# Optimization experiments

Measured on AMD Instinct MI355X. Metric: run time of the kernel, lower is better.

The kernel has to match this reference:

```python
import jax, jax.numpy as jnp
import numpy as np

N_TF, N_GENES, W, FANIN, B = 1024, 20000, 4, 16, 128
M = N_GENES * W  # middle width = 80000


def _build_edges(rng):
    # layer 1: each of the M per-gene nodes draws FANIN random TF inputs
    out1 = np.repeat(np.arange(M, dtype=np.int32), FANIN)
    in1 = rng.integers(0, N_TF, size=M * FANIN).astype(np.int32)
    in1[-1] = N_TF - 1  # ensure full input dim is touched
    # layer 2: dense WxW block per gene (node i of gene g sees all W nodes of gene g)
    out2 = np.repeat(np.arange(M, dtype=np.int32), W)
    gene = np.arange(M, dtype=np.int32) // W
    in2 = (gene[:, None] * W + np.arange(W, dtype=np.int32)[None, :]).reshape(-1)
    # layer 3: each gene output sums its W nodes
    out3 = np.repeat(np.arange(N_GENES, dtype=np.int32), W)
    in3 = np.arange(M, dtype=np.int32)
    return out1, in1, out2, in2, out3, in3


def setup_inputs() -> dict:
    key = jax.random.key(0)
    ks = jax.random.split(key, 7)
    rng = np.random.default_rng(0)
    out1, in1, out2, in2, out3, in3 = _build_edges(rng)
    scale1 = 1.0 / np.sqrt(FANIN)
    scale2 = 1.0 / np.sqrt(W)
    return {
        "features": jax.random.normal(ks[0], (B, N_TF), jnp.float32),
        "w1": jax.random.normal(ks[1], (out1.shape[0],), jnp.float32) * scale1,
        "b1": jax.random.normal(ks[2], (M,), jnp.float32) * 0.01,
        "w2": jax.random.normal(ks[3], (out2.shape[0],), jnp.float32) * scale2,
        "b2": jax.random.normal(ks[4], (M,), jnp.float32) * 0.01,
        "w3": jax.random.normal(ks[5], (out3.shape[0],), jnp.float32) * scale2,
        "b3": jax.random.normal(ks[6], (N_GENES,), jnp.float32) * 0.01,
        "out1": jnp.asarray(out1), "in1": jnp.asarray(in1),
        "out2": jnp.asarray(out2), "in2": jnp.asarray(in2),
        "out3": jnp.asarray(out3), "in3": jnp.asarray(in3),
    }


def _sparse_linear(x, w, b, out_idx, in_idx):
    # x: [B, n_in]; per-edge gather-multiply-scatter, y[b, o] = sum_e w_e * x[b, in_e] + b_o
    contrib = x.T[in_idx] * w[:, None]                      # [nnz, B]
    y = jax.ops.segment_sum(contrib, out_idx, num_segments=b.shape[0])  # [n_out, B]
    return y.T + b


def reference(features, w1, b1, w2, b2, w3, b3, out1, in1, out2, in2, out3, in3):
    h = jnp.tanh(_sparse_linear(features, w1, b1, out1, in1))
    h = jnp.tanh(_sparse_linear(h, w2, b2, out2, in2))
    return _sparse_linear(h, w3, b3, out3, in3)  # [B, N_GENES]
```

## Files before the change

### kernel.cpp

```cpp
#include <hip/hip_runtime.h>
#include <hip/hip_fp16.h>

#define N_TF    1024
#define N_GENES 20000
#define WW      4
#define FANIN   16
#define BATCH   128
#define EPG     (WW * FANIN)
#define NNZ1    (N_GENES * EPG)

#define GPB      16
#define NTHREADS 1024
#define NBLK     (N_GENES / GPB)
#define YROW     (BATCH + 2)

typedef unsigned int uint32;

__device__ __forceinline__ float2 fast_tanh2(float a, float b) {
    const float ta = __expf(2.0f * a);
    const float tb = __expf(2.0f * b);
    const float da = ta + 1.0f;
    const float db = tb + 1.0f;
    const float r  = __builtin_amdgcn_rcpf(da * db);
    return make_float2(fmaf(-2.0f * db, r, 1.0f),
                       fmaf(-2.0f * da, r, 1.0f));
}

__global__ __launch_bounds__(256) void transpose_cvt_kernel(
    const float* __restrict__ in, __half* __restrict__ out)
{
    __shared__ float tile[32][33];
    const int bx = blockIdx.x;
    const int by = blockIdx.y;
    const int tx = threadIdx.x;
    const int ty = threadIdx.y;
#pragma unroll
    for (int k = 0; k < 32; k += 8)
        tile[ty + k][tx] = in[(by * 32 + ty + k) * N_TF + bx * 32 + tx];
    __syncthreads();
    const int b = by * 32 + tx;
#pragma unroll
    for (int k = 0; k < 32; k += 8) {
        const int tf = bx * 32 + ty + k;
        out[tf * BATCH + b] = __float2half(tile[tx][ty + k]);
    }
}

__global__ __launch_bounds__(NTHREADS, 4) void fused_kernel(
    const __half* __restrict__ xh,
    const int*    __restrict__ in1,
    const float*  __restrict__ w1,
    const float*  __restrict__ b1,
    const float*  __restrict__ w2,
    const float*  __restrict__ b2,
    const float*  __restrict__ w3,
    const float*  __restrict__ b3,
    float*        __restrict__ out)
{
    __shared__ float yt[GPB * YROW];

    const int tid  = threadIdx.x;
    const int wid  = __builtin_amdgcn_readfirstlane(tid >> 6);
    const int lane = tid & 63;
    const int g    = blockIdx.x * GPB + wid;
    const int voff = lane << 2;
    const char* xb = (const char*)xh;

    const uint4*  __restrict__ ig = (const uint4*)(in1 + g * EPG);
    const float4* __restrict__ wg = (const float4*)(w1 + g * EPG);

    __half2 acc[WW];
    const __half2 hz = __float2half2_rn(0.0f);
#pragma unroll
    for (int i = 0; i < WW; ++i) acc[i] = hz;

#pragma unroll
    for (int half = 0; half < 2; ++half) {
        uint32 idx[32];
        float  wsc[32];
#pragma unroll
        for (int k = 0; k < 8; ++k) {
            const uint4  iq = ig[half * 8 + k];
            const float4 wq = wg[half * 8 + k];
            idx[k * 4 + 0] = iq.x;  idx[k * 4 + 1] = iq.y;
            idx[k * 4 + 2] = iq.z;  idx[k * 4 + 3] = iq.w;
            wsc[k * 4 + 0] = wq.x;  wsc[k * 4 + 1] = wq.y;
            wsc[k * 4 + 2] = wq.z;  wsc[k * 4 + 3] = wq.w;
        }
        __half2 xv[32];
#pragma unroll
        for (int t = 0; t < 32; ++t)
            xv[t] = *(const __half2*)(xb + (((size_t)idx[t]) << 8) + voff);
#pragma unroll
        for (int t = 0; t < 32; ++t) {
            const __half2 wd = __float2half2_rn(wsc[t]);
            const int tt = half * 32 + t;
            acc[tt >> 4] = __hfma2(wd, xv[t], acc[tt >> 4]);
        }
    }

    float2 h1[WW];
#pragma unroll
    for (int i = 0; i < WW; ++i) {
        const float  bb = b1[g * WW + i];
        const float2 af = __half22float2(acc[i]);
        h1[i] = fast_tanh2(af.x + bb, af.y + bb);
    }

    float2 h2[WW];
#pragma unroll
    for (int i = 0; i < WW; ++i) {
        const float4 w  = *(const float4*)(w2 + g * 16 + i * 4);
        const float  bb = b2[g * WW + i];
        const float sx = bb + w.x * h1[0].x + w.y * h1[1].x
                            + w.z * h1[2].x + w.w * h1[3].x;
        const float sy = bb + w.x * h1[0].y + w.y * h1[1].y
                            + w.z * h1[2].y + w.w * h1[3].y;
        h2[i] = fast_tanh2(sx, sy);
    }

    const float4 wv3 = *(const float4*)(w3 + g * 4);
    const float  bv  = b3[g];
    const float yx = bv + wv3.x * h2[0].x + wv3.y * h2[1].x
                        + wv3.z * h2[2].x + wv3.w * h2[3].x;
    const float yy = bv + wv3.x * h2[0].y + wv3.y * h2[1].y
                        + wv3.z * h2[2].y + wv3.w * h2[3].y;

    float2* ytw = (float2*)(yt + wid * YROW);
    ytw[lane] = make_float2(yx, yy);

    __syncthreads();

    const int g0 = blockIdx.x * GPB;
#pragma unroll
    for (int it = 0; it < (BATCH * GPB) / NTHREADS; ++it) {
        const int idx = it * NTHREADS + tid;
        const int gq  = idx & (GPB - 1);
        const int b   = idx >> 4;
        out[b * N_GENES + g0 + gq] = yt[gq * YROW + b];
    }
}

extern "C" void kernel_launch(void* const* d_in, const int* in_sizes, int n_in,
                              void* d_out, int out_size, void* d_ws, size_t ws_size,
                              hipStream_t stream)
{
    const float* features = (const float*)d_in[0];
    const float* w1 = (const float*)d_in[1];
    const float* b1 = (const float*)d_in[2];
    const float* w2 = (const float*)d_in[3];
    const float* b2 = (const float*)d_in[4];
    const float* w3 = (const float*)d_in[5];
    const float* b3 = (const float*)d_in[6];
    const int*   in1 = (const int*)d_in[8];
    float* out = (float*)d_out;

    __half* xh = (__half*)d_ws;

    hipLaunchKernelGGL(transpose_cvt_kernel, dim3(32, 4), dim3(32, 8), 0, stream,
                       features, xh);
    hipLaunchKernelGGL(fused_kernel, dim3(NBLK), dim3(NTHREADS), 0, stream,
                       xh, in1, w1, b1, w2, b2, w3, b3, out);
}
```

Measured before the change: 112.1 us.

## Stage half-batch feature table in LDS and gather from shared memory

The feature matrix is split into two batch halves in the transposed fp16 layout. Each block copies one half (128 KB) into LDS and processes about 78 genes in a persistent loop over waves. Each wave handles two edges per instruction by splitting its lanes into two 32-lane groups and combines the partial sums with a cross-lane shuffle. This replaces random global/L2 gathers with LDS gathers. In exchange it adds a per-block 128 KB copy (512 blocks means 64 MB of total LDS fill traffic) and limits occupancy to one block per CU, which reduces latency hiding.

Measured after the change: 138.7 us. +23.7%, slower.

```diff
diff --git a/kernel.cpp b/kernel.cpp
--- a/kernel.cpp
+++ b/kernel.cpp
@@ -6,13 +6,17 @@
 #define WW      4
 #define FANIN   16
 #define BATCH   128
+#define HALF_B  64
 #define EPG     (WW * FANIN)
-#define NNZ1    (N_GENES * EPG)
 
-#define GPB      16
 #define NTHREADS 1024
-#define NBLK     (N_GENES / GPB)
-#define YROW     (BATCH + 2)
+#define NWAVES   16
+#define NBLK     512
+#define MAXG     80
+#define YROW     65
+#define XH_BYTES (N_TF * HALF_B * 2)
+#define YT_BYTES (MAXG * YROW * 4)
+#define LDS_BYTES (XH_BYTES + YT_BYTES)
 
 typedef unsigned int uint32;
 
@@ -38,16 +42,18 @@
     for (int k = 0; k < 32; k += 8)
         tile[ty + k][tx] = in[(by * 32 + ty + k) * N_TF + bx * 32 + tx];
     __syncthreads();
-    const int b = by * 32 + tx;
+    const int b  = by * 32 + tx;
+    const int h  = b >> 6;
+    const int bl = b & 63;
 #pragma unroll
     for (int k = 0; k < 32; k += 8) {
         const int tf = bx * 32 + ty + k;
-        out[tf * BATCH + b] = __float2half(tile[tx][ty + k]);
+        out[h * (N_TF * HALF_B) + tf * HALF_B + bl] = __float2half(tile[tx][ty + k]);
     }
 }
 
-__global__ __launch_bounds__(NTHREADS, 4) void fused_kernel(
-    const __half* __restrict__ xh,
+__global__ __launch_bounds__(NTHREADS) void fused_kernel(
+    const __half* __restrict__ xhs,
     const int*    __restrict__ in1,
     const float*  __restrict__ w1,
     const float*  __restrict__ b1,
@@ -57,87 +63,108 @@
     const float*  __restrict__ b3,
     float*        __restrict__ out)
 {
-    __shared__ float yt[GPB * YROW];
+    extern __shared__ char smem[];
+    __half* xh = (__half*)smem;
+    float*  yt = (float*)(smem + XH_BYTES);
 
-    const int tid  = threadIdx.x;
+    const int tid = threadIdx.x;
+    const int bx  = blockIdx.x;
+    const int h   = bx & 1;
+    const int gb  = bx >> 1;
+    const int g0  = gb * 78 + (gb < 32 ? gb : 32);
+    const int ng  = 78 + (gb < 32 ? 1 : 0);
+
+    {
+        const uint4* __restrict__ src = (const uint4*)(xhs + h * (N_TF * HALF_B));
+        uint4* dst = (uint4*)xh;
+#pragma unroll
+        for (int i = 0; i < (XH_BYTES / 16) / NTHREADS; ++i)
+            dst[i * NTHREADS + tid] = src[i * NTHREADS + tid];
+    }
+    __syncthreads();
+
     const int wid  = __builtin_amdgcn_readfirstlane(tid >> 6);
     const int lane = tid & 63;
-    const int g    = blockIdx.x * GPB + wid;
-    const int voff = lane << 2;
-    const char* xb = (const char*)xh;
+    const int lsel = lane >> 5;
+    const int ll   = (lane & 31) << 2;
 
-    const uint4*  __restrict__ ig = (const uint4*)(in1 + g * EPG);
-    const float4* __restrict__ wg = (const float4*)(w1 + g * EPG);
+    for (int gl = wid; gl < ng; gl += NWAVES) {
+        const int g = g0 + gl;
+        const uint4*  __restrict__ ig = (const uint4*)(in1 + g * EPG);
+        const float4* __restrict__ wg = (const float4*)(w1 + g * EPG);
 
-    __half2 acc[WW];
-    const __half2 hz = __float2half2_rn(0.0f);
+        float2 h1[WW];
 #pragma unroll
-    for (int i = 0; i < WW; ++i) acc[i] = hz;
+        for (int node = 0; node < WW; ++node) {
+            __half2 xv[8], wv[8];
+#pragma unroll
+            for (int kk = 0; kk < 4; ++kk) {
+                const uint4  iq = ig[node * 4 + kk];
+                const float4 wq = wg[node * 4 + kk];
+                {
+                    const int offA = (int)(iq.x << 7);
+                    const int offB = (int)(iq.y << 7);
+                    const int off  = lsel ? offB : offA;
+                    xv[2 * kk] = *(const __half2*)((const char*)xh + off + ll);
+                    const float wf = lsel ? wq.y : wq.x;
+                    wv[2 * kk] = __float2half2_rn(wf);
+                }
+                {
+                    const int offA = (int)(iq.z << 7);
+                    const int offB = (int)(iq.w << 7);
+                    const int off  = lsel ? offB : offA;
+                    xv[2 * kk + 1] = *(const __half2*)((const char*)xh + off + ll);
+                    const float wf = lsel ? wq.w : wq.z;
+                    wv[2 * kk + 1] = __float2half2_rn(wf);
+                }
+            }
+            __half2 acc = __float2half2_rn(0.0f);
+#pragma unroll
+            for (int t = 0; t < 8; ++t)
+                acc = __hfma2(wv[t], xv[t], acc);
+            int ai;  __builtin_memcpy(&ai, &acc, 4);
+            const int oi = __shfl_xor(ai, 32, 64);
+            __half2 other;  __builtin_memcpy(&other, &oi, 4);
+            const float2 af = __half22float2(acc);
+            const float2 of = __half22float2(other);
+            const float  bb = b1[g * WW + node];
+            h1[node] = fast_tanh2(af.x + of.x + bb, af.y + of.y + bb);
+        }
+
+        float2 h2[WW];
+#pragma unroll
+        for (int i = 0; i < WW; ++i) {
+            const float4 w  = *(const float4*)(w2 + g * 16 + i * 4);
+            const float  bb = b2[g * WW + i];
+            const float sx = bb + w.x * h1[0].x + w.y * h1[1].x
+                                + w.z * h1[2].x + w.w * h1[3].x;
+            const float sy = bb + w.x * h1[0].y + w.y * h1[1].y
+                                + w.z * h1[2].y + w.w * h1[3].y;
+            h2[i] = fast_tanh2(sx, sy);
+        }
+
+        const float4 wv3 = *(const float4*)(w3 + g * 4);
+        const float  bv  = b3[g];
+        const float yx = bv + wv3.x * h2[0].x + wv3.y * h2[1].x
+                            + wv3.z * h2[2].x + wv3.w * h2[3].x;
+        const float yy = bv + wv3.x * h2[0].y + wv3.y * h2[1].y
+                            + wv3.z * h2[2].y + wv3.w * h2[3].y;
+
+        if (lsel == 0) {
+            const int q = lane & 31;
+            float* yp = yt + gl * YROW + 2 * q;
+            yp[0] = yx;
+            yp[1] = yy;
+        }
+    }
+    __syncthreads();
 
 #pragma unroll
-    for (int half = 0; half < 2; ++half) {
-        uint32 idx[32];
-        float  wsc[32];
-#pragma unroll
-        for (int k = 0; k < 8; ++k) {
-            const uint4  iq = ig[half * 8 + k];
-            const float4 wq = wg[half * 8 + k];
-            idx[k * 4 + 0] = iq.x;  idx[k * 4 + 1] = iq.y;
-            idx[k * 4 + 2] = iq.z;  idx[k * 4 + 3] = iq.w;
-            wsc[k * 4 + 0] = wq.x;  wsc[k * 4 + 1] = wq.y;
-            wsc[k * 4 + 2] = wq.z;  wsc[k * 4 + 3] = wq.w;
-        }
-        __half2 xv[32];
-#pragma unroll
-        for (int t = 0; t < 32; ++t)
-            xv[t] = *(const __half2*)(xb + (((size_t)idx[t]) << 8) + voff);
-#pragma unroll
-        for (int t = 0; t < 32; ++t) {
-            const __half2 wd = __float2half2_rn(wsc[t]);
-            const int tt = half * 32 + t;
-            acc[tt >> 4] = __hfma2(wd, xv[t], acc[tt >> 4]);
-        }
-    }
-
-    float2 h1[WW];
-#pragma unroll
-    for (int i = 0; i < WW; ++i) {
-        const float  bb = b1[g * WW + i];
-        const float2 af = __half22float2(acc[i]);
-        h1[i] = fast_tanh2(af.x + bb, af.y + bb);
-    }
-
-    float2 h2[WW];
-#pragma unroll
-    for (int i = 0; i < WW; ++i) {
-        const float4 w  = *(const float4*)(w2 + g * 16 + i * 4);
-        const float  bb = b2[g * WW + i];
-        const float sx = bb + w.x * h1[0].x + w.y * h1[1].x
-                            + w.z * h1[2].x + w.w * h1[3].x;
-        const float sy = bb + w.x * h1[0].y + w.y * h1[1].y
-                            + w.z * h1[2].y + w.w * h1[3].y;
-        h2[i] = fast_tanh2(sx, sy);
-    }
-
-    const float4 wv3 = *(const float4*)(w3 + g * 4);
-    const float  bv  = b3[g];
-    const float yx = bv + wv3.x * h2[0].x + wv3.y * h2[1].x
-                        + wv3.z * h2[2].x + wv3.w * h2[3].x;
-    const float yy = bv + wv3.x * h2[0].y + wv3.y * h2[1].y
-                        + wv3.z * h2[2].y + wv3.w * h2[3].y;
-
-    float2* ytw = (float2*)(yt + wid * YROW);
-    ytw[lane] = make_float2(yx, yy);
-
-    __syncthreads();
-
-    const int g0 = blockIdx.x * GPB;
-#pragma unroll
-    for (int it = 0; it < (BATCH * GPB) / NTHREADS; ++it) {
-        const int idx = it * NTHREADS + tid;
-        const int gq  = idx & (GPB - 1);
-        const int b   = idx >> 4;
-        out[b * N_GENES + g0 + gq] = yt[gq * YROW + b];
+    for (int r = 0; r < HALF_B / NWAVES; ++r) {
+        const int bb  = r * NWAVES + wid;
+        const int row = (h * HALF_B + bb) * N_GENES + g0;
+        for (int gl = lane; gl < ng; gl += 64)
+            out[row + gl] = yt[gl * YROW + bb];
     }
 }
 
@@ -155,10 +182,10 @@
     const int*   in1 = (const int*)d_in[8];
     float* out = (float*)d_out;
 
-    __half* xh = (__half*)d_ws;
+    __half* xhs = (__half*)d_ws;
 
     hipLaunchKernelGGL(transpose_cvt_kernel, dim3(32, 4), dim3(32, 8), 0, stream,
-                       features, xh);
-    hipLaunchKernelGGL(fused_kernel, dim3(NBLK), dim3(NTHREADS), 0, stream,
-                       xh, in1, w1, b1, w2, b2, w3, b3, out);
+                       features, xhs);
+    hipLaunchKernelGGL(fused_kernel, dim3(NBLK), dim3(NTHREADS), LDS_BYTES, stream,
+                       xhs, in1, w1, b1, w2, b2, w3, b3, out);
 }
```

## Quantize features to per-TF uint8 and fold scale/offset into layer-1 weights

Applied to the files above, without the earlier changes.

Replaces the fp16 transposed feature copy with per-TF min/max asymmetric 8-bit quantization, which halves the bytes fetched by each gathered load in the fused kernel. A new prep kernel folds each TF's scale into the layer-1 weights and its offset into the layer-1 bias. Layer-1 accumulation becomes fp32 FMAs on byte-to-float conversions instead of half2 FMAs. In exchange it adds a kernel launch and an extra pass that reads in1/w1 and writes a scaled weight array every call, and 8-bit quantization may loosen accuracy.

Result: slower. 118.4 us (+5.6%).

```diff
diff --git a/kernel.cpp b/kernel.cpp
--- a/kernel.cpp
+++ b/kernel.cpp
@@ -7,6 +7,7 @@
 #define FANIN   16
 #define BATCH   128
 #define EPG     (WW * FANIN)
+#define MM      (N_GENES * WW)
 #define NNZ1    (N_GENES * EPG)
 
 #define GPB      16
@@ -26,31 +27,82 @@
                        fmaf(-2.0f * da, r, 1.0f));
 }
 
-__global__ __launch_bounds__(256) void transpose_cvt_kernel(
-    const float* __restrict__ in, __half* __restrict__ out)
-{
-    __shared__ float tile[32][33];
-    const int bx = blockIdx.x;
-    const int by = blockIdx.y;
-    const int tx = threadIdx.x;
-    const int ty = threadIdx.y;
-#pragma unroll
-    for (int k = 0; k < 32; k += 8)
-        tile[ty + k][tx] = in[(by * 32 + ty + k) * N_TF + bx * 32 + tx];
-    __syncthreads();
-    const int b = by * 32 + tx;
-#pragma unroll
-    for (int k = 0; k < 32; k += 8) {
-        const int tf = bx * 32 + ty + k;
-        out[tf * BATCH + b] = __float2half(tile[tx][ty + k]);
-    }
-}
-
-__global__ __launch_bounds__(NTHREADS, 4) void fused_kernel(
-    const __half* __restrict__ xh,
+__device__ __forceinline__ float cvt_ub0(uint32 v) {
+#if __has_builtin(__builtin_amdgcn_cvt_f32_ubyte0)
+    return __builtin_amdgcn_cvt_f32_ubyte0(v);
+#else
+    return (float)(v & 0xffu);
+#endif
+}
+__device__ __forceinline__ float cvt_ub1(uint32 v) {
+#if __has_builtin(__builtin_amdgcn_cvt_f32_ubyte1)
+    return __builtin_amdgcn_cvt_f32_ubyte1(v);
+#else
+    return (float)((v >> 8) & 0xffu);
+#endif
+}
+
+__global__ __launch_bounds__(512) void prep1_kernel(
+    const float* __restrict__ features,
+    unsigned char* __restrict__ xu,
+    float2*       __restrict__ so)
+{
+    const int wid  = threadIdx.x >> 6;
+    const int lane = threadIdx.x & 63;
+    const int tf   = blockIdx.x * 8 + wid;
+
+    const float a = features[(2 * lane)     * N_TF + tf];
+    const float b = features[(2 * lane + 1) * N_TF + tf];
+    float mn = fminf(a, b), mx = fmaxf(a, b);
+#pragma unroll
+    for (int off = 1; off < 64; off <<= 1) {
+        mn = fminf(mn, __shfl_xor(mn, off, 64));
+        mx = fmaxf(mx, __shfl_xor(mx, off, 64));
+    }
+    const float range = fmaxf(mx - mn, 1e-20f);
+    const float inv   = 255.0f / range;
+    const float s     = range * (1.0f / 255.0f);
+
+    float va = fmaf(a - mn, inv, 0.5f);
+    float vb = fmaf(b - mn, inv, 0.5f);
+    va = fminf(fmaxf(va, 0.0f), 255.0f);
+    vb = fminf(fmaxf(vb, 0.0f), 255.0f);
+    const uint32 ua = (uint32)va;
+    const uint32 ub = (uint32)vb;
+    *(unsigned short*)(xu + tf * BATCH + 2 * lane) =
+        (unsigned short)(ua | (ub << 8));
+
+    if (lane == 0) so[tf] = make_float2(s, mn);
+}
+
+__global__ __launch_bounds__(256) void prep2_kernel(
     const int*    __restrict__ in1,
     const float*  __restrict__ w1,
     const float*  __restrict__ b1,
+    const float2* __restrict__ so,
+    float*        __restrict__ w1s,
+    float*        __restrict__ b1p)
+{
+    const int n = blockIdx.x * 256 + threadIdx.x;
+    if (n >= MM) return;
+    float corr = 0.0f;
+#pragma unroll
+    for (int j = 0; j < FANIN; ++j) {
+        const int    e   = n * FANIN + j;
+        const int    idx = in1[e];
+        const float  w   = w1[e];
+        const float2 p   = so[idx];
+        w1s[e] = w * p.x;
+        corr  = fmaf(w, p.y, corr);
+    }
+    b1p[n] = b1[n] + corr;
+}
+
+__global__ __launch_bounds__(NTHREADS, 4) void fused_kernel(
+    const unsigned char* __restrict__ xu,
+    const int*    __restrict__ in1,
+    const float*  __restrict__ w1s,
+    const float*  __restrict__ b1p,
     const float*  __restrict__ w2,
     const float*  __restrict__ b2,
     const float*  __restrict__ w3,
@@ -63,16 +115,15 @@
     const int wid  = __builtin_amdgcn_readfirstlane(tid >> 6);
     const int lane = tid & 63;
     const int g    = blockIdx.x * GPB + wid;
-    const int voff = lane << 2;
-    const char* xb = (const char*)xh;
+    const int voff = lane << 1;
+    const char* xb = (const char*)xu;
 
     const uint4*  __restrict__ ig = (const uint4*)(in1 + g * EPG);
-    const float4* __restrict__ wg = (const float4*)(w1 + g * EPG);
-
-    __half2 acc[WW];
-    const __half2 hz = __float2half2_rn(0.0f);
-#pragma unroll
-    for (int i = 0; i < WW; ++i) acc[i] = hz;
+    const float4* __restrict__ wg = (const float4*)(w1s + g * EPG);
+
+    float2 acc[WW];
+#pragma unroll
+    for (int i = 0; i < WW; ++i) acc[i] = make_float2(0.0f, 0.0f);
 
 #pragma unroll
     for (int half = 0; half < 2; ++half) {
@@ -87,24 +138,27 @@
             wsc[k * 4 + 0] = wq.x;  wsc[k * 4 + 1] = wq.y;
             wsc[k * 4 + 2] = wq.z;  wsc[k * 4 + 3] = wq.w;
         }
-        __half2 xv[32];
+        unsigned short xv[32];
 #pragma unroll
         for (int t = 0; t < 32; ++t)
-            xv[t] = *(const __half2*)(xb + (((size_t)idx[t]) << 8) + voff);
+            xv[t] = *(const unsigned short*)(xb + (((size_t)idx[t]) << 7) + voff);
 #pragma unroll
         for (int t = 0; t < 32; ++t) {
-            const __half2 wd = __float2half2_rn(wsc[t]);
+            const uint32 v  = (uint32)xv[t];
+            const float  x0 = cvt_ub0(v);
+            const float  x1 = cvt_ub1(v);
             const int tt = half * 32 + t;
-            acc[tt >> 4] = __hfma2(wd, xv[t], acc[tt >> 4]);
+            const int nd = tt >> 4;
+            acc[nd].x = fmaf(wsc[t], x0, acc[nd].x);
+            acc[nd].y = fmaf(wsc[t], x1, acc[nd].y);
         }
     }
 
     float2 h1[WW];
 #pragma unroll
     for (int i = 0; i < WW; ++i) {
-        const float  bb = b1[g * WW + i];
-        const float2 af = __half22float2(acc[i]);
-        h1[i] = fast_tanh2(af.x + bb, af.y + bb);
+        const float bb = b1p[g * WW + i];
+        h1[i] = fast_tanh2(acc[i].x + bb, acc[i].y + bb);
     }
 
     float2 h2[WW];
@@ -155,10 +209,15 @@
     const int*   in1 = (const int*)d_in[8];
     float* out = (float*)d_out;
 
-    __half* xh = (__half*)d_ws;
-
-    hipLaunchKernelGGL(transpose_cvt_kernel, dim3(32, 4), dim3(32, 8), 0, stream,
-                       features, xh);
+    unsigned char* xu  = (unsigned char*)d_ws;
+    float2*        so  = (float2*)((char*)d_ws + (size_t)N_TF * BATCH);
+    float*         w1s = (float*)((char*)so + (size_t)N_TF * sizeof(float2));
+    float*         b1p = w1s + NNZ1;
+
+    hipLaunchKernelGGL(prep1_kernel, dim3(N_TF / 8), dim3(512), 0, stream,
+                       features, xu, so);
+    hipLaunchKernelGGL(prep2_kernel, dim3((MM + 255) / 256), dim3(256), 0, stream,
+                       in1, w1, b1, so, w1s, b1p);
     hipLaunchKernelGGL(fused_kernel, dim3(NBLK), dim3(NTHREADS), 0, stream,
-                       xh, in1, w1, b1, w2, b2, w3, b3, out);
-}
+                       xu, in1, w1s, b1p, w2, b2, w3, b3, out);
+}
```
